# Kernel tuning notes

Measured on AMD Instinct MI355X. Metric: run time of the kernel, lower is better.

The kernel has to match this reference:

```python
import jax, jax.numpy as jnp
import numpy as np

P = 5; G = 60; E = 256; H = 8
NPD = G // P; NP = NPD ** 3          # 1728 patch tokens
LE = 4; LD = 2; NC = 40; B = 4
MASK_RATIO = 0.75
NUM_MASK = int(MASK_RATIO * NP)      # 1296 masked, 432 visible


def setup_inputs() -> dict:
    key = jax.random.key(0)
    ki = iter(jax.random.split(key, 64))
    def n(shape, s=0.02):
        return jax.random.normal(next(ki), shape, jnp.float32) * s
    d = {
        "x": jax.random.normal(next(ki), (B, 1, G, G, G), jnp.float32),
        "noise": jax.random.uniform(next(ki), (B, NP), jnp.float32),
        "patch_w": n((E, 1, P, P, P), 0.05),
        "patch_b": jnp.zeros((E,), jnp.float32),
        "pos_embed": n((1, NP, E)),
        "dec_pos_embed": n((1, NP, E)),
        "mask_token": n((1, 1, E)),
        "pred_w": n((P ** 3, E)),
        "pred_b": jnp.zeros((P ** 3,), jnp.float32),
        "cls_w": n((NC, E)),
        "cls_b": jnp.zeros((NC,), jnp.float32),
    }
    for pre, L in (("enc", LE), ("dec", LD)):
        d[pre + "_qkv_w"] = n((L, 3 * E, E)); d[pre + "_qkv_b"] = jnp.zeros((L, 3 * E), jnp.float32)
        d[pre + "_out_w"] = n((L, E, E));     d[pre + "_out_b"] = jnp.zeros((L, E), jnp.float32)
        d[pre + "_ln1_w"] = jnp.ones((L, E), jnp.float32); d[pre + "_ln1_b"] = jnp.zeros((L, E), jnp.float32)
        d[pre + "_ln2_w"] = jnp.ones((L, E), jnp.float32); d[pre + "_ln2_b"] = jnp.zeros((L, E), jnp.float32)
        d[pre + "_ffn1_w"] = n((L, 4 * E, E)); d[pre + "_ffn1_b"] = jnp.zeros((L, 4 * E), jnp.float32)
        d[pre + "_ffn2_w"] = n((L, E, 4 * E)); d[pre + "_ffn2_b"] = jnp.zeros((L, E), jnp.float32)
    return d


def _ln(x, w, b):
    m = x.mean(-1, keepdims=True)
    v = ((x - m) ** 2).mean(-1, keepdims=True)
    return (x - m) / jnp.sqrt(v + 1e-5) * w + b


def _layer(x, qkv_w, qkv_b, out_w, out_b, l1w, l1b, l2w, l2b, f1w, f1b, f2w, f2b):
    # post-norm TransformerEncoderLayer with exact-erf GELU (dropout=0 at eval)
    Bx, S, Ex = x.shape
    dh = Ex // H
    qkv = x @ qkv_w.T + qkv_b                      # [B,S,3E]
    q, k, v = jnp.split(qkv, 3, axis=-1)
    q = q.reshape(Bx, S, H, dh); k = k.reshape(Bx, S, H, dh); v = v.reshape(Bx, S, H, dh)
    scores = jnp.einsum('bqhd,bkhd->bhqk', q, k) / np.float32(np.sqrt(dh))
    attn = jax.nn.softmax(scores, axis=-1)
    o = jnp.einsum('bhqk,bkhd->bqhd', attn, v).reshape(Bx, S, Ex)
    x = _ln(x + o @ out_w.T + out_b, l1w, l1b)
    f = jax.nn.gelu(x @ f1w.T + f1b, approximate=False) @ f2w.T + f2b
    return _ln(x + f, l2w, l2b)


def _stack(x, params, L):
    for i in range(L):
        x = _layer(x, *(a[i] for a in params))
    return x


def _forward(x, noise, patch_w, patch_b, pos_embed, dec_pos_embed, mask_token,
             enc_qkv_w, enc_qkv_b, enc_out_w, enc_out_b, enc_ln1_w, enc_ln1_b, enc_ln2_w, enc_ln2_b,
             enc_ffn1_w, enc_ffn1_b, enc_ffn2_w, enc_ffn2_b,
             dec_qkv_w, dec_qkv_b, dec_out_w, dec_out_b, dec_ln1_w, dec_ln1_b, dec_ln2_w, dec_ln2_b,
             dec_ffn1_w, dec_ffn1_b, dec_ffn2_w, dec_ffn2_b,
             pred_w, pred_b, cls_w, cls_b):
    Bx = x.shape[0]
    # patchify: [B,1,G,G,G] -> [B, NP, P^3]
    xg = x.reshape(Bx, 1, NPD, P, NPD, P, NPD, P)
    xg = xg.transpose(0, 2, 4, 6, 1, 3, 5, 7).reshape(Bx, NP, P ** 3)
    # Conv3d with stride == kernel == patch embedding over flattened patches
    tokens = xg @ patch_w.reshape(E, P ** 3).T + patch_b + pos_embed   # [B,NP,E]
    # random masking
    ids_shuffle = jnp.argsort(noise, axis=1)
    ids_mask = ids_shuffle[:, :NUM_MASK]
    ids_keep = ids_shuffle[:, NUM_MASK:]                                # [B, 432]
    mask = jnp.zeros((Bx, NP), x.dtype).at[jnp.arange(Bx)[:, None], ids_mask].set(1.0)
    x_vis = jnp.take_along_axis(tokens, ids_keep[:, :, None], axis=1)   # [B,432,E]
    enc = _stack(x_vis,
                 (enc_qkv_w, enc_qkv_b, enc_out_w, enc_out_b, enc_ln1_w, enc_ln1_b,
                  enc_ln2_w, enc_ln2_b, enc_ffn1_w, enc_ffn1_b, enc_ffn2_w, enc_ffn2_b), LE)
    cls_logits = enc.mean(axis=1) @ cls_w.T + cls_b
    # scatter encoded tokens back into full mask-token buffer (vectorized over batch)
    x_dec = jnp.broadcast_to(mask_token, (Bx, NP, E))
    x_dec = jax.vmap(lambda base, ids, e: base.at[ids].set(e))(x_dec, ids_keep, enc)
    dec = _stack(x_dec + dec_pos_embed,
                 (dec_qkv_w, dec_qkv_b, dec_out_w, dec_out_b, dec_ln1_w, dec_ln1_b,
                  dec_ln2_w, dec_ln2_b, dec_ffn1_w, dec_ffn1_b, dec_ffn2_w, dec_ffn2_b), LD)
    pred = dec @ pred_w.T + pred_b                                      # [B,NP,P^3]
    return pred, xg, mask, cls_logits


def reference(x, noise, patch_w, patch_b, pos_embed, dec_pos_embed, mask_token,
              enc_qkv_w, enc_qkv_b, enc_out_w, enc_out_b, enc_ln1_w, enc_ln1_b, enc_ln2_w, enc_ln2_b,
              enc_ffn1_w, enc_ffn1_b, enc_ffn2_w, enc_ffn2_b,
              dec_qkv_w, dec_qkv_b, dec_out_w, dec_out_b, dec_ln1_w, dec_ln1_b, dec_ln2_w, dec_ln2_b,
              dec_ffn1_w, dec_ffn1_b, dec_ffn2_w, dec_ffn2_b,
              pred_w, pred_b, cls_w, cls_b):
    return _forward(x, noise, patch_w, patch_b, pos_embed, dec_pos_embed, mask_token,
                    enc_qkv_w, enc_qkv_b, enc_out_w, enc_out_b, enc_ln1_w, enc_ln1_b, enc_ln2_w, enc_ln2_b,
                    enc_ffn1_w, enc_ffn1_b, enc_ffn2_w, enc_ffn2_b,
                    dec_qkv_w, dec_qkv_b, dec_out_w, dec_out_b, dec_ln1_w, dec_ln1_b, dec_ln2_w, dec_ln2_b,
                    dec_ffn1_w, dec_ffn1_b, dec_ffn2_w, dec_ffn2_b,
                    pred_w, pred_b, cls_w, cls_b)
```

## Files before the change

### kernel.cpp

```cpp
#include <hip/hip_runtime.h>
#include <hip/hip_bf16.h>
#include <math.h>

#define E 256
#define Hh 8
#define DH 32
#define NP 1728
#define PP3 125
#define Bb 4
#define NUM_MASKC 1296
#define NKEEP 432
#define LE 4
#define LD 2
#define NC 40

typedef __attribute__((ext_vector_type(4))) float f32x4;
typedef __attribute__((ext_vector_type(8))) short bf16x8;
typedef __attribute__((ext_vector_type(4))) short s16x4;

#define QSCALE 0.25505654708402214f

__device__ inline short f2b(float f) {
    __hip_bfloat16 h = __float2bfloat16(f);
    return *reinterpret_cast<short*>(&h);
}
__device__ inline float b2f(short s) {
    union { unsigned u; float f; } v; v.u = ((unsigned)(unsigned short)s) << 16;
    return v.f;
}
__device__ inline unsigned cvt_pk(float lo, float hi) {
    unsigned r;
    asm("v_cvt_pk_bf16_f32 %0, %1, %2" : "=v"(r) : "v"(lo), "v"(hi));
    return r;
}

struct W2B { const float* src; short* dst; int n; };
struct W2BTab { W2B e[25]; };
__global__ void k_w2b(W2BTab tab) {
    W2B w = tab.e[blockIdx.y];
    int i = (blockIdx.x*256 + threadIdx.x) * 8;
    if (i + 8 <= w.n) {
        float4 a = *(const float4*)(w.src + i);
        float4 b = *(const float4*)(w.src + i + 4);
        short t[8] = {f2b(a.x),f2b(a.y),f2b(a.z),f2b(a.w),
                      f2b(b.x),f2b(b.y),f2b(b.z),f2b(b.w)};
        *(bf16x8*)(w.dst + i) = *(const bf16x8*)t;
    }
}

__global__ void k_rank(const float* __restrict__ noise, int* __restrict__ shuf,
                       int* __restrict__ keep_pos, float* __restrict__ out_mask)
{
    __shared__ float ns[NP];
    int b = blockIdx.x / 7, it = blockIdx.x % 7;
    const float* nr = noise + (size_t)b*NP;
    int tid = threadIdx.x;
    for (int j = tid; j < NP; j += 256) ns[j] = nr[j];
    __syncthreads();
    int i = it*256 + tid;
    if (i < NP) {
        float ni = ns[i];
        int rank = 0;
        for (int j = 0; j < NP; ++j) {
            float nj = ns[j];
            rank += (nj < ni) || (nj == ni && j < i);
        }
        shuf[b*NP + rank] = i;
        keep_pos[b*NP + i] = (rank >= NUM_MASKC) ? (rank - NUM_MASKC) : -1;
        out_mask[b*NP + i] = (rank < NUM_MASKC) ? 1.0f : 0.0f;
    }
}

__global__ void k_xg(const float* __restrict__ x, float* __restrict__ out_xg)
{
    int bn = blockIdx.x;
    int b = bn / NP, n = bn % NP;
    int a0 = n / 144, r = n % 144, b0 = r / 12, c0 = r % 12;
    int t = threadIdx.x;
    if (t < PP3) {
        int pa = t / 25, rem = t % 25, pbq = rem / 5, pc = rem % 5;
        out_xg[(size_t)bn*PP3 + t] =
            x[(size_t)b*216000 + (size_t)(a0*5+pa)*3600 + (b0*5+pbq)*60 + (c0*5+pc)];
    }
}

__global__ void k_patch_vis(const float* __restrict__ x, const float* __restrict__ pw,
                            const float* __restrict__ pb, const float* __restrict__ pos,
                            const int* __restrict__ shuf, short* __restrict__ visb)
{
    int row = blockIdx.x;
    int b = row / NKEEP, s = row % NKEEP;
    int n = shuf[b*NP + NUM_MASKC + s];
    int a0 = n / 144, r = n % 144, b0 = r / 12, c0 = r % 12;
    __shared__ float patch[PP3];
    int t = threadIdx.x;
    if (t < PP3) {
        int pa = t / 25, rem = t % 25, pbq = rem / 5, pc = rem % 5;
        patch[t] = x[(size_t)b*216000 + (size_t)(a0*5+pa)*3600 + (b0*5+pbq)*60 + (c0*5+pc)];
    }
    __syncthreads();
    float acc = pb[t] + pos[(size_t)n*E + t];
    const float* w = pw + (size_t)t*PP3;
    for (int k = 0; k < PP3; ++k) acc += patch[k] * w[k];
    visb[(size_t)row*E + t] = f2b(acc);
}

__global__ __launch_bounds__(256) void
k_mgemm(const short* __restrict__ A, const short* __restrict__ W,
        const float* __restrict__ bias, float* __restrict__ Cf,
        short* __restrict__ Cb, int M, int N, int K, int act,
        short* __restrict__ qkvb, short* __restrict__ vTb, int S)
{
    __shared__ short As[64][72];
    __shared__ short Ws[64][72];
    int tid = threadIdx.x;
    int lane = tid & 63, wave = tid >> 6;
    int rb = blockIdx.y * 64, cb = blockIdx.x * 64;
    int wr = (wave >> 1) * 32, wc = (wave & 1) * 32;
    int fr = lane & 15, fq = lane >> 4;
    f32x4 acc[2][2];
    #pragma unroll
    for (int m = 0; m < 2; ++m)
        #pragma unroll
        for (int n = 0; n < 2; ++n) acc[m][n] = (f32x4)0.f;
    int sr = tid >> 2;
    int sk = (tid & 3) * 16;
    for (int kk0 = 0; kk0 < K; kk0 += 64) {
        {
            int gr = rb + sr;
            if (gr < M) {
                const short* s = A + (size_t)gr*K + kk0 + sk;
                *(bf16x8*)&As[sr][sk]     = *(const bf16x8*)s;
                *(bf16x8*)&As[sr][sk + 8] = *(const bf16x8*)(s + 8);
            } else {
                *(bf16x8*)&As[sr][sk]     = (bf16x8)0;
                *(bf16x8*)&As[sr][sk + 8] = (bf16x8)0;
            }
            int gc = cb + sr;
            if (gc < N) {
                const short* s = W + (size_t)gc*K + kk0 + sk;
                *(bf16x8*)&Ws[sr][sk]     = *(const bf16x8*)s;
                *(bf16x8*)&Ws[sr][sk + 8] = *(const bf16x8*)(s + 8);
            } else {
                *(bf16x8*)&Ws[sr][sk]     = (bf16x8)0;
                *(bf16x8*)&Ws[sr][sk + 8] = (bf16x8)0;
            }
        }
        __syncthreads();
        #pragma unroll
        for (int kk = 0; kk < 64; kk += 32) {
            int ko = kk + 8*fq;
            bf16x8 a0 = *(const bf16x8*)&As[wr + fr][ko];
            bf16x8 a1 = *(const bf16x8*)&As[wr + 16 + fr][ko];
            bf16x8 b0 = *(const bf16x8*)&Ws[wc + fr][ko];
            bf16x8 b1 = *(const bf16x8*)&Ws[wc + 16 + fr][ko];
            acc[0][0] = __builtin_amdgcn_mfma_f32_16x16x32_bf16(a0, b0, acc[0][0], 0, 0, 0);
            acc[0][1] = __builtin_amdgcn_mfma_f32_16x16x32_bf16(a0, b1, acc[0][1], 0, 0, 0);
            acc[1][0] = __builtin_amdgcn_mfma_f32_16x16x32_bf16(a1, b0, acc[1][0], 0, 0, 0);
            acc[1][1] = __builtin_amdgcn_mfma_f32_16x16x32_bf16(a1, b1, acc[1][1], 0, 0, 0);
        }
        __syncthreads();
    }
    #pragma unroll
    for (int m = 0; m < 2; ++m) {
        #pragma unroll
        for (int n = 0; n < 2; ++n) {
            int col = cb + wc + n*16 + fr;
            if (col >= N) continue;
            float bv = bias[col];
            #pragma unroll
            for (int r = 0; r < 4; ++r) {
                int row = rb + wr + m*16 + fq*4 + r;
                if (row >= M) continue;
                float v = acc[m][n][r] + bv;
                if (act == 1) v = 0.5f * v * (1.f + erff(v * 0.70710678118654752f));
                if (qkvb) {
                    if (col < 512) {
                        if (col < 256) v *= QSCALE;
                        qkvb[(size_t)row*768 + col] = f2b(v);
                    } else {
                        int b = row / S, s = row - b*S;
                        int hd = col - 512;
                        vTb[((size_t)(b*Hh + (hd >> 5))*DH + (hd & 31))*S + s] = f2b(v);
                    }
                } else if (Cb) {
                    Cb[(size_t)row*N + col] = f2b(v);
                } else {
                    Cf[(size_t)row*N + col] = v;
                }
            }
        }
    }
}

__global__ __launch_bounds__(128) void
k_fattn(const short* __restrict__ qkvb, const short* __restrict__ vTb,
        short* __restrict__ o, int S)
{
    __shared__ short Ks[64][40];
    __shared__ short Vt[32][72];
    int nqt = (S + 31) >> 5;
    int bi = blockIdx.x;
    int qt = bi % nqt, bh = bi / nqt;
    int h = bh & 7, b = bh >> 3;
    int q0 = qt << 5;
    int tid = threadIdx.x;
    int lane = tid & 63, wave = tid >> 6;
    int fr = lane & 15, fq = lane >> 4;
    bf16x8 qfrag = (bf16x8)0;
    int qg = q0 + wave*16 + fr;
    if (qg < S)
        qfrag = *(const bf16x8*)(qkvb + (size_t)(b*S+qg)*768 + h*DH + 8*fq);
    f32x4 acc0 = (f32x4)0.f, acc1 = (f32x4)0.f;
    float lpart = 0.f;
    int krow = tid >> 1, kh = (tid & 1) * 16;
    int vrow = tid >> 2, vk4 = (tid & 3) * 16;
    const short* vTh = vTb + (size_t)bh*DH*S;
    int src1 = fr + ((fq & 1) << 5);
    int src2 = src1 + 16;
    bool sel = (fq >> 1) != 0;
    for (int kt0 = 0; kt0 < S; kt0 += 64) {
        {
            int kg = kt0 + krow;
            if (kg < S) {
                const short* src = qkvb + (size_t)(b*S+kg)*768 + 256 + h*DH + kh;
                *(bf16x8*)&Ks[krow][kh]     = *(const bf16x8*)src;
                *(bf16x8*)&Ks[krow][kh + 8] = *(const bf16x8*)(src + 8);
            } else {
                *(bf16x8*)&Ks[krow][kh]     = (bf16x8)0;
                *(bf16x8*)&Ks[krow][kh + 8] = (bf16x8)0;
            }
            if (kt0 + vk4 < S) {
                const short* vs = vTh + (size_t)vrow*S + kt0 + vk4;
                *(bf16x8*)&Vt[vrow][vk4]     = *(const bf16x8*)vs;
                *(bf16x8*)&Vt[vrow][vk4 + 8] = *(const bf16x8*)(vs + 8);
            } else {
                *(bf16x8*)&Vt[vrow][vk4]     = (bf16x8)0;
                *(bf16x8*)&Vt[vrow][vk4 + 8] = (bf16x8)0;
            }
        }
        __syncthreads();
        f32x4 st[4];
        #pragma unroll
        for (int kt = 0; kt < 4; ++kt) {
            bf16x8 kf = *(const bf16x8*)&Ks[kt*16 + fr][8*fq];
            st[kt] = __builtin_amdgcn_mfma_f32_16x16x32_bf16(kf, qfrag, (f32x4)0.f, 0, 0, 0);
        }
        if (kt0 + 64 > S) {
            #pragma unroll
            for (int kt = 0; kt < 4; ++kt)
                #pragma unroll
                for (int r = 0; r < 4; ++r)
                    if (kt0 + kt*16 + 4*fq + r >= S) st[kt][r] = -1e30f;
        }
        float tsum = 0.f;
        unsigned pk[4][2];
        #pragma unroll
        for (int kt = 0; kt < 4; ++kt) {
            float p0 = exp2f(st[kt][0]), p1 = exp2f(st[kt][1]);
            float p2 = exp2f(st[kt][2]), p3 = exp2f(st[kt][3]);
            tsum += (p0 + p1) + (p2 + p3);
            pk[kt][0] = cvt_pk(p0, p1);
            pk[kt][1] = cvt_pk(p2, p3);
        }
        lpart += tsum;
        #pragma unroll
        for (int t = 0; t < 2; ++t) {
            unsigned a0 = __shfl(pk[2*t][0], src1),   a1 = __shfl(pk[2*t][1], src1);
            unsigned a2 = __shfl(pk[2*t][0], src2),   a3 = __shfl(pk[2*t][1], src2);
            unsigned b0 = __shfl(pk[2*t+1][0], src1), b1 = __shfl(pk[2*t+1][1], src1);
            unsigned b2 = __shfl(pk[2*t+1][0], src2), b3 = __shfl(pk[2*t+1][1], src2);
            union { unsigned u[4]; bf16x8 v; } B2;
            B2.u[0] = sel ? b0 : a0;
            B2.u[1] = sel ? b1 : a1;
            B2.u[2] = sel ? b2 : a2;
            B2.u[3] = sel ? b3 : a3;
            bf16x8 v0 = *(const bf16x8*)&Vt[fr][t*32 + 8*fq];
            bf16x8 v1 = *(const bf16x8*)&Vt[16 + fr][t*32 + 8*fq];
            acc0 = __builtin_amdgcn_mfma_f32_16x16x32_bf16(v0, B2.v, acc0, 0, 0, 0);
            acc1 = __builtin_amdgcn_mfma_f32_16x16x32_bf16(v1, B2.v, acc1, 0, 0, 0);
        }
        __syncthreads();
    }
    float lsum = lpart;
    lsum += __shfl_xor(lsum, 16);
    lsum += __shfl_xor(lsum, 32);
    if (qg < S) {
        float inv = 1.f / lsum;
        short* op = o + (size_t)(b*S + qg)*E + h*DH;
        s16x4 o0 = { f2b(acc0[0]*inv), f2b(acc0[1]*inv), f2b(acc0[2]*inv), f2b(acc0[3]*inv) };
        s16x4 o1 = { f2b(acc1[0]*inv), f2b(acc1[1]*inv), f2b(acc1[2]*inv), f2b(acc1[3]*inv) };
        *(s16x4*)&op[4*fq]      = o0;
        *(s16x4*)&op[16 + 4*fq] = o1;
    }
}

__global__ __launch_bounds__(256) void
k_lnadd(short* __restrict__ x, const short* __restrict__ rsd,
        const float* __restrict__ w, const float* __restrict__ bv)
{
    int row = blockIdx.x*4 + (threadIdx.x >> 6);
    int lane = threadIdx.x & 63;
    int c0 = lane * 4;
    size_t base = (size_t)row*E + c0;
    s16x4 xv = *(const s16x4*)&x[base];
    s16x4 rv = *(const s16x4*)&rsd[base];
    float v[4];
    float s = 0.f, sq = 0.f;
    #pragma unroll
    for (int j = 0; j < 4; ++j) {
        v[j] = b2f(xv[j]) + b2f(rv[j]);
        s += v[j]; sq += v[j]*v[j];
    }
    #pragma unroll
    for (int off = 1; off < 64; off <<= 1) {
        s  += __shfl_xor(s, off);
        sq += __shfl_xor(sq, off);
    }
    float mean = s * (1.f/E);
    float var = fmaxf(sq * (1.f/E) - mean*mean, 0.f);
    float rstd = 1.f / sqrtf(var + 1e-5f);
    float4 wv = *(const float4*)&w[c0];
    float4 bb = *(const float4*)&bv[c0];
    s16x4 o;
    o[0] = f2b((v[0]-mean)*rstd*wv.x + bb.x);
    o[1] = f2b((v[1]-mean)*rstd*wv.y + bb.y);
    o[2] = f2b((v[2]-mean)*rstd*wv.z + bb.z);
    o[3] = f2b((v[3]-mean)*rstd*wv.w + bb.w);
    *(s16x4*)&x[base] = o;
}

__global__ void k_mean(const short* __restrict__ xv, float* __restrict__ mb)
{
    int b = blockIdx.x, tid = threadIdx.x;
    float s = 0.f;
    for (int r = 0; r < NKEEP; ++r) s += b2f(xv[((size_t)b*NKEEP + r)*E + tid]);
    mb[b*E + tid] = s * (1.f/NKEEP);
}

__global__ void k_cls(const float* __restrict__ mb, const float* __restrict__ cw,
                      const float* __restrict__ cb, float* __restrict__ out)
{
    int t = threadIdx.x;
    if (t < Bb*NC) {
        int b = t / NC, c = t % NC;
        float acc = cb[c];
        for (int k = 0; k < E; ++k) acc += mb[b*E+k]*cw[c*E+k];
        out[t] = acc;
    }
}

__global__ void k_scatter(const short* __restrict__ visb, const int* __restrict__ keep_pos,
                          const float* __restrict__ mtok, const float* __restrict__ dpos,
                          short* __restrict__ xdb)
{
    int bn = blockIdx.x; int b = bn / NP, n = bn % NP;
    int t = threadIdx.x;
    int s = keep_pos[bn];
    float base = (s >= 0) ? b2f(visb[((size_t)b*NKEEP + s)*E + t]) : mtok[t];
    xdb[(size_t)bn*E + t] = f2b(base + dpos[(size_t)n*E + t]);
}

extern "C" void kernel_launch(void* const* d_in, const int* in_sizes, int n_in,
                              void* d_out, int out_size, void* d_ws, size_t ws_size,
                              hipStream_t stream)
{
    const float* x        = (const float*)d_in[0];
    const float* noise    = (const float*)d_in[1];
    const float* patch_w  = (const float*)d_in[2];
    const float* patch_b  = (const float*)d_in[3];
    const float* pos      = (const float*)d_in[4];
    const float* dpos     = (const float*)d_in[5];
    const float* mtok     = (const float*)d_in[6];
    const float* pred_w   = (const float*)d_in[7];
    const float* pred_b   = (const float*)d_in[8];
    const float* cls_w    = (const float*)d_in[9];
    const float* cls_b    = (const float*)d_in[10];
    const float* enc_w[12]; for (int i = 0; i < 12; ++i) enc_w[i] = (const float*)d_in[11+i];
    const float* dec_w[12]; for (int i = 0; i < 12; ++i) dec_w[i] = (const float*)d_in[23+i];

    float* out = (float*)d_out;
    float* out_pred = out;
    float* out_xg   = out + 864000;
    float* out_mask = out + 1728000;
    float* out_cls  = out + 1734912;

    short* S0   = (short*)d_ws;
    short* qkvb = S0;
    short* bigb = qkvb + 5308416;
    short* vTb  = bigb + 7077888;
    short* visb = vTb  + 1769472;
    short* xdb  = visb + 442368;
    short* c1b  = xdb  + 1769472;
    short* c2b  = c1b  + 1769472;
    short* wb   = c2b  + 1769472;
    float* mb   = (float*)(wb + 4750592);
    int* shuf   = (int*)(mb + 1024);
    int* keep   = shuf + Bb*NP;

    const int LSTRIDE = 786432;
    W2BTab tab;
    int wi = 0;
    size_t off = 0;
    auto addw = [&](const float* src, int n) {
        tab.e[wi].src = src; tab.e[wi].dst = wb + off; tab.e[wi].n = n;
        ++wi; off += n;
    };
    for (int l = 0; l < LE; ++l) {
        addw(enc_w[0] + (size_t)l*3*E*E, 3*E*E);
        addw(enc_w[2] + (size_t)l*E*E,   E*E);
        addw(enc_w[8] + (size_t)l*4*E*E, 4*E*E);
        addw(enc_w[10]+ (size_t)l*4*E*E, 4*E*E);
    }
    for (int l = 0; l < LD; ++l) {
        addw(dec_w[0] + (size_t)l*3*E*E, 3*E*E);
        addw(dec_w[2] + (size_t)l*E*E,   E*E);
        addw(dec_w[8] + (size_t)l*4*E*E, 4*E*E);
        addw(dec_w[10]+ (size_t)l*4*E*E, 4*E*E);
    }
    addw(pred_w, PP3*E);
    hipLaunchKernelGGL(k_w2b, dim3(128, 25), dim3(256), 0, stream, tab);

    auto gemm = [&](const short* A, const short* W, const float* bias,
                    float* Cf, short* Cb, int M, int N, int K, int act,
                    short* qb, short* vb, int Sv) {
        dim3 g((N+63)/64, (M+63)/64);
        hipLaunchKernelGGL(k_mgemm, g, dim3(256), 0, stream, A, W, bias,
                           Cf, Cb, M, N, K, act, qb, vb, Sv);
    };

    auto layer = [&](short* xbuf, int Bl, int S, const float* const* Wp,
                     const short* wbase, int l) {
        int M = Bl * S;
        int nqt = (S + 31) / 32;
        const short* wq = wbase + (size_t)l*LSTRIDE;
        const short* wo = wq + 3*E*E;
        const short* w1 = wo + E*E;
        const short* w2 = w1 + 4*E*E;
        gemm(xbuf, wq, Wp[1] + l*3*E, nullptr, nullptr, M, 3*E, E, 0, qkvb, vTb, S);
        k_fattn<<<Bl*Hh*nqt, 128, 0, stream>>>(qkvb, vTb, c1b, S);
        gemm(c1b, wo, Wp[3] + l*E, nullptr, c2b, M, E, E, 0, nullptr, nullptr, 1);
        k_lnadd<<<M/4, 256, 0, stream>>>(xbuf, c2b, Wp[4] + l*E, Wp[5] + l*E);
        gemm(xbuf, w1, Wp[9] + l*4*E, nullptr, bigb, M, 4*E, E, 1, nullptr, nullptr, 1);
        gemm(bigb, w2, Wp[11] + l*E, nullptr, c2b, M, E, 4*E, 0, nullptr, nullptr, 1);
        k_lnadd<<<M/4, 256, 0, stream>>>(xbuf, c2b, Wp[6] + l*E, Wp[7] + l*E);
    };

    k_rank<<<Bb*7, 256, 0, stream>>>(noise, shuf, keep, out_mask);
    k_xg<<<Bb*NP, 128, 0, stream>>>(x, out_xg);
    k_patch_vis<<<Bb*NKEEP, 256, 0, stream>>>(x, patch_w, patch_b, pos, shuf, visb);

    const short* enc_wb = wb;
    const short* dec_wb = wb + (size_t)LE*LSTRIDE;
    const short* pred_wb = wb + (size_t)(LE+LD)*LSTRIDE;

    for (int l = 0; l < LE; ++l) layer(visb, Bb, NKEEP, enc_w, enc_wb, l);

    k_mean<<<Bb, 256, 0, stream>>>(visb, mb);
    k_cls<<<1, 256, 0, stream>>>(mb, cls_w, cls_b, out_cls);

    k_scatter<<<Bb*NP, 256, 0, stream>>>(visb, keep, mtok, dpos, xdb);
    for (int l = 0; l < LD; ++l) layer(xdb, Bb, NP, dec_w, dec_wb, l);
    gemm(xdb, pred_wb, pred_b, out_pred, nullptr, Bb*NP, PP3, E, 0, nullptr, nullptr, 1);
}
```

Before: 637.0 us.

## Use direct global-to-LDS loads with XOR swizzle in GEMM, double-buffer attention K/V

The GEMM tile loads now use global_load_lds to write straight into LDS without passing through registers. The tiles use an XOR-swizzled layout with no padding to avoid bank conflicts. The bounds checks are dropped, so the prediction weight is zero-padded to 128 rows to make out-of-range W reads safe. The attention kernel double-buffers its K/V tiles, prefetching the next tile into registers during compute, which removes one barrier per iteration. A risk is that A rows past M, for example 432*4 visible-token GEMMs not divisible by 64, are read without a guard and may go beyond the buffer.

```diff
diff --git a/kernel.cpp b/kernel.cpp
--- a/kernel.cpp
+++ b/kernel.cpp
@@ -33,8 +33,13 @@
     asm("v_cvt_pk_bf16_f32 %0, %1, %2" : "=v"(r) : "v"(lo), "v"(hi));
     return r;
 }
-
-struct W2B { const float* src; short* dst; int n; };
+__device__ inline void gl_lds16(const void* g, void* l) {
+    __builtin_amdgcn_global_load_lds(
+        (const __attribute__((address_space(1))) void*)g,
+        (__attribute__((address_space(3))) void*)l, 16, 0, 0);
+}
+
+struct W2B { const float* src; short* dst; int n; int npad; };
 struct W2BTab { W2B e[25]; };
 __global__ void k_w2b(W2BTab tab) {
     W2B w = tab.e[blockIdx.y];
@@ -45,6 +50,8 @@
         short t[8] = {f2b(a.x),f2b(a.y),f2b(a.z),f2b(a.w),
                       f2b(b.x),f2b(b.y),f2b(b.z),f2b(b.w)};
         *(bf16x8*)(w.dst + i) = *(const bf16x8*)t;
+    } else if (i < w.npad) {
+        *(bf16x8*)(w.dst + i) = (bf16x8)0;
     }
 }
 
@@ -111,8 +118,8 @@
         short* __restrict__ Cb, int M, int N, int K, int act,
         short* __restrict__ qkvb, short* __restrict__ vTb, int S)
 {
-    __shared__ short As[64][72];
-    __shared__ short Ws[64][72];
+    __shared__ short As[64][64];
+    __shared__ short Ws[64][64];
     int tid = threadIdx.x;
     int lane = tid & 63, wave = tid >> 6;
     int rb = blockIdx.y * 64, cb = blockIdx.x * 64;
@@ -123,37 +130,25 @@
     for (int m = 0; m < 2; ++m)
         #pragma unroll
         for (int n = 0; n < 2; ++n) acc[m][n] = (f32x4)0.f;
-    int sr = tid >> 2;
-    int sk = (tid & 3) * 16;
+    int rl = lane >> 3, cl = lane & 7;
+    int r0 = 16 * wave;
     for (int kk0 = 0; kk0 < K; kk0 += 64) {
-        {
-            int gr = rb + sr;
-            if (gr < M) {
-                const short* s = A + (size_t)gr*K + kk0 + sk;
-                *(bf16x8*)&As[sr][sk]     = *(const bf16x8*)s;
-                *(bf16x8*)&As[sr][sk + 8] = *(const bf16x8*)(s + 8);
-            } else {
-                *(bf16x8*)&As[sr][sk]     = (bf16x8)0;
-                *(bf16x8*)&As[sr][sk + 8] = (bf16x8)0;
-            }
-            int gc = cb + sr;
-            if (gc < N) {
-                const short* s = W + (size_t)gc*K + kk0 + sk;
-                *(bf16x8*)&Ws[sr][sk]     = *(const bf16x8*)s;
-                *(bf16x8*)&Ws[sr][sk + 8] = *(const bf16x8*)(s + 8);
-            } else {
-                *(bf16x8*)&Ws[sr][sk]     = (bf16x8)0;
-                *(bf16x8*)&Ws[sr][sk + 8] = (bf16x8)0;
-            }
+        #pragma unroll
+        for (int j = 0; j < 2; ++j) {
+            int r = r0 + 8*j + rl;
+            int cs = cl ^ (r & 7);
+            gl_lds16(A + (size_t)(rb + r)*K + kk0 + cs*8, &As[r0 + 8*j][0]);
+            gl_lds16(W + (size_t)(cb + r)*K + kk0 + cs*8, &Ws[r0 + 8*j][0]);
         }
         __syncthreads();
         #pragma unroll
-        for (int kk = 0; kk < 64; kk += 32) {
-            int ko = kk + 8*fq;
-            bf16x8 a0 = *(const bf16x8*)&As[wr + fr][ko];
-            bf16x8 a1 = *(const bf16x8*)&As[wr + 16 + fr][ko];
-            bf16x8 b0 = *(const bf16x8*)&Ws[wc + fr][ko];
-            bf16x8 b1 = *(const bf16x8*)&Ws[wc + 16 + fr][ko];
+        for (int t = 0; t < 2; ++t) {
+            int rA0 = wr + fr, rA1 = wr + 16 + fr;
+            int rB0 = wc + fr, rB1 = wc + 16 + fr;
+            bf16x8 a0 = *(const bf16x8*)&As[rA0][(((4*t + fq) ^ (rA0 & 7)) << 3)];
+            bf16x8 a1 = *(const bf16x8*)&As[rA1][(((4*t + fq) ^ (rA1 & 7)) << 3)];
+            bf16x8 b0 = *(const bf16x8*)&Ws[rB0][(((4*t + fq) ^ (rB0 & 7)) << 3)];
+            bf16x8 b1 = *(const bf16x8*)&Ws[rB1][(((4*t + fq) ^ (rB1 & 7)) << 3)];
             acc[0][0] = __builtin_amdgcn_mfma_f32_16x16x32_bf16(a0, b0, acc[0][0], 0, 0, 0);
             acc[0][1] = __builtin_amdgcn_mfma_f32_16x16x32_bf16(a0, b1, acc[0][1], 0, 0, 0);
             acc[1][0] = __builtin_amdgcn_mfma_f32_16x16x32_bf16(a1, b0, acc[1][0], 0, 0, 0);
@@ -197,8 +192,8 @@
 k_fattn(const short* __restrict__ qkvb, const short* __restrict__ vTb,
         short* __restrict__ o, int S)
 {
-    __shared__ short Ks[64][40];
-    __shared__ short Vt[32][72];
+    __shared__ short Ks[2][64][40];
+    __shared__ short Vt[2][32][72];
     int nqt = (S + 31) >> 5;
     int bi = blockIdx.x;
     int qt = bi % nqt, bh = bi / nqt;
@@ -219,31 +214,37 @@
     int src1 = fr + ((fq & 1) << 5);
     int src2 = src1 + 16;
     bool sel = (fq >> 1) != 0;
-    for (int kt0 = 0; kt0 < S; kt0 += 64) {
-        {
-            int kg = kt0 + krow;
-            if (kg < S) {
-                const short* src = qkvb + (size_t)(b*S+kg)*768 + 256 + h*DH + kh;
-                *(bf16x8*)&Ks[krow][kh]     = *(const bf16x8*)src;
-                *(bf16x8*)&Ks[krow][kh + 8] = *(const bf16x8*)(src + 8);
-            } else {
-                *(bf16x8*)&Ks[krow][kh]     = (bf16x8)0;
-                *(bf16x8*)&Ks[krow][kh + 8] = (bf16x8)0;
-            }
-            if (kt0 + vk4 < S) {
-                const short* vs = vTh + (size_t)vrow*S + kt0 + vk4;
-                *(bf16x8*)&Vt[vrow][vk4]     = *(const bf16x8*)vs;
-                *(bf16x8*)&Vt[vrow][vk4 + 8] = *(const bf16x8*)(vs + 8);
-            } else {
-                *(bf16x8*)&Vt[vrow][vk4]     = (bf16x8)0;
-                *(bf16x8*)&Vt[vrow][vk4 + 8] = (bf16x8)0;
-            }
-        }
-        __syncthreads();
+    int nt = (S + 63) >> 6;
+    bf16x8 kr0, kr1, vr0, vr1;
+    auto LOAD = [&](int t) {
+        int kg = (t << 6) + krow;
+        if (kg < S) {
+            const short* src = qkvb + (size_t)(b*S+kg)*768 + 256 + h*DH + kh;
+            kr0 = *(const bf16x8*)src;
+            kr1 = *(const bf16x8*)(src + 8);
+        } else { kr0 = (bf16x8)0; kr1 = (bf16x8)0; }
+        if ((t << 6) + vk4 < S) {
+            const short* vs = vTh + (size_t)vrow*S + (t << 6) + vk4;
+            vr0 = *(const bf16x8*)vs;
+            vr1 = *(const bf16x8*)(vs + 8);
+        } else { vr0 = (bf16x8)0; vr1 = (bf16x8)0; }
+    };
+    auto WRITE = [&](int p) {
+        *(bf16x8*)&Ks[p][krow][kh]      = kr0;
+        *(bf16x8*)&Ks[p][krow][kh + 8]  = kr1;
+        *(bf16x8*)&Vt[p][vrow][vk4]     = vr0;
+        *(bf16x8*)&Vt[p][vrow][vk4 + 8] = vr1;
+    };
+    LOAD(0); WRITE(0);
+    __syncthreads();
+    for (int t = 0; t < nt; ++t) {
+        int p = t & 1;
+        int kt0 = t << 6;
+        if (t + 1 < nt) LOAD(t + 1);
         f32x4 st[4];
         #pragma unroll
         for (int kt = 0; kt < 4; ++kt) {
-            bf16x8 kf = *(const bf16x8*)&Ks[kt*16 + fr][8*fq];
+            bf16x8 kf = *(const bf16x8*)&Ks[p][kt*16 + fr][8*fq];
             st[kt] = __builtin_amdgcn_mfma_f32_16x16x32_bf16(kf, qfrag, (f32x4)0.f, 0, 0, 0);
         }
         if (kt0 + 64 > S) {
@@ -265,21 +266,22 @@
         }
         lpart += tsum;
         #pragma unroll
-        for (int t = 0; t < 2; ++t) {
-            unsigned a0 = __shfl(pk[2*t][0], src1),   a1 = __shfl(pk[2*t][1], src1);
-            unsigned a2 = __shfl(pk[2*t][0], src2),   a3 = __shfl(pk[2*t][1], src2);
-            unsigned b0 = __shfl(pk[2*t+1][0], src1), b1 = __shfl(pk[2*t+1][1], src1);
-            unsigned b2 = __shfl(pk[2*t+1][0], src2), b3 = __shfl(pk[2*t+1][1], src2);
+        for (int t2 = 0; t2 < 2; ++t2) {
+            unsigned a0 = __shfl(pk[2*t2][0], src1),   a1 = __shfl(pk[2*t2][1], src1);
+            unsigned a2 = __shfl(pk[2*t2][0], src2),   a3 = __shfl(pk[2*t2][1], src2);
+            unsigned b0 = __shfl(pk[2*t2+1][0], src1), b1 = __shfl(pk[2*t2+1][1], src1);
+            unsigned b2 = __shfl(pk[2*t2+1][0], src2), b3 = __shfl(pk[2*t2+1][1], src2);
             union { unsigned u[4]; bf16x8 v; } B2;
             B2.u[0] = sel ? b0 : a0;
             B2.u[1] = sel ? b1 : a1;
             B2.u[2] = sel ? b2 : a2;
             B2.u[3] = sel ? b3 : a3;
-            bf16x8 v0 = *(const bf16x8*)&Vt[fr][t*32 + 8*fq];
-            bf16x8 v1 = *(const bf16x8*)&Vt[16 + fr][t*32 + 8*fq];
+            bf16x8 v0 = *(const bf16x8*)&Vt[p][fr][t2*32 + 8*fq];
+            bf16x8 v1 = *(const bf16x8*)&Vt[p][16 + fr][t2*32 + 8*fq];
             acc0 = __builtin_amdgcn_mfma_f32_16x16x32_bf16(v0, B2.v, acc0, 0, 0, 0);
             acc1 = __builtin_amdgcn_mfma_f32_16x16x32_bf16(v1, B2.v, acc1, 0, 0, 0);
         }
+        if (t + 1 < nt) WRITE(p ^ 1);
         __syncthreads();
     }
     float lsum = lpart;
@@ -394,7 +396,7 @@
     short* c1b  = xdb  + 1769472;
     short* c2b  = c1b  + 1769472;
     short* wb   = c2b  + 1769472;
-    float* mb   = (float*)(wb + 4750592);
+    float* mb   = (float*)(wb + 4751360);
     int* shuf   = (int*)(mb + 1024);
     int* keep   = shuf + Bb*NP;
 
@@ -402,23 +404,24 @@
     W2BTab tab;
     int wi = 0;
     size_t off = 0;
-    auto addw = [&](const float* src, int n) {
-        tab.e[wi].src = src; tab.e[wi].dst = wb + off; tab.e[wi].n = n;
-        ++wi; off += n;
+    auto addw = [&](const float* src, int n, int npad) {
+        tab.e[wi].src = src; tab.e[wi].dst = wb + off;
+        tab.e[wi].n = n; tab.e[wi].npad = npad;
+        ++wi; off += npad;
     };
     for (int l = 0; l < LE; ++l) {
-        addw(enc_w[0] + (size_t)l*3*E*E, 3*E*E);
-        addw(enc_w[2] + (size_t)l*E*E,   E*E);
-        addw(enc_w[8] + (size_t)l*4*E*E, 4*E*E);
-        addw(enc_w[10]+ (size_t)l*4*E*E, 4*E*E);
+        addw(enc_w[0] + (size_t)l*3*E*E, 3*E*E, 3*E*E);
+        addw(enc_w[2] + (size_t)l*E*E,   E*E,   E*E);
+        addw(enc_w[8] + (size_t)l*4*E*E, 4*E*E, 4*E*E);
+        addw(enc_w[10]+ (size_t)l*4*E*E, 4*E*E, 4*E*E);
     }
     for (int l = 0; l < LD; ++l) {
-        addw(dec_w[0] + (size_t)l*3*E*E, 3*E*E);
-        addw(dec_w[2] + (size_t)l*E*E,   E*E);
-        addw(dec_w[8] + (size_t)l*4*E*E, 4*E*E);
-        addw(dec_w[10]+ (size_t)l*4*E*E, 4*E*E);
-    }
-    addw(pred_w, PP3*E);
+        addw(dec_w[0] + (size_t)l*3*E*E, 3*E*E, 3*E*E);
+        addw(dec_w[2] + (size_t)l*E*E,   E*E,   E*E);
+        addw(dec_w[8] + (size_t)l*4*E*E, 4*E*E, 4*E*E);
+        addw(dec_w[10]+ (size_t)l*4*E*E, 4*E*E, 4*E*E);
+    }
+    addw(pred_w, PP3*E, 128*E);
     hipLaunchKernelGGL(k_w2b, dim3(128, 25), dim3(256), 0, stream, tab);
 
     auto gemm = [&](const short* A, const short* W, const float* bias,
```

After: 560.8 us. 1.14x faster.
